# Kernel tuning notes

Hardware: AMD Instinct MI355X
Metric: run time of the kernel (lower is better)

## Reference

```python
import jax, jax.numpy as jnp
import numpy as np

B = 16384      # batch of (user, item) interactions
N = 819200     # total packed implicit-history items (~50 per user)
U = 100000     # num_users
I = 100000     # num_items
D = 64         # emb_dim


def setup_inputs() -> dict:
    key = jax.random.key(0)
    ks = jax.random.split(key, 8)
    user_ids = jax.random.randint(ks[0], (B,), 0, U)
    item_ids = jax.random.randint(ks[1], (B,), 0, I)
    offsets = jnp.sort(jax.random.randint(ks[2], (B,), 0, N)).at[0].set(0)
    flat_implicit = jax.random.randint(ks[3], (N,), 0, I)
    user_emb = 0.1 * jax.random.normal(ks[4], (U, D), dtype=jnp.float32)
    item_emb = 0.1 * jax.random.normal(ks[5], (I, D), dtype=jnp.float32)
    implicit_item_emb = 0.1 * jax.random.normal(ks[6], (I, D), dtype=jnp.float32)
    user_bias = jnp.zeros((U, 1), dtype=jnp.float32)
    item_bias = jnp.zeros((I, 1), dtype=jnp.float32)
    global_bias = jnp.zeros((1,), dtype=jnp.float32)
    return {"user_ids": user_ids, "item_ids": item_ids, "offsets": offsets,
            "flat_implicit": flat_implicit, "user_emb": user_emb,
            "item_emb": item_emb, "implicit_item_emb": implicit_item_emb,
            "user_bias": user_bias, "item_bias": item_bias,
            "global_bias": global_bias}


def reference(user_ids, item_ids, offsets, flat_implicit, user_emb, item_emb,
              implicit_item_emb, user_bias, item_bias, global_bias):
    n = flat_implicit.shape[0]
    b = offsets.shape[0]
    u = user_emb[user_ids]                       # [B, D]
    i = item_emb[item_ids]                       # [B, D]
    imp = implicit_item_emb[flat_implicit]       # [N, D]
    # ragged segment ids from start offsets (empty segments get no rows)
    seg_ids = jnp.searchsorted(offsets, jnp.arange(n), side="right") - 1
    summed = jax.ops.segment_sum(imp, seg_ids, num_segments=b)  # [B, D]
    sizes = jnp.diff(jnp.concatenate([offsets, jnp.array([n], dtype=offsets.dtype)]))
    norm = jnp.where(sizes > 0, jnp.sqrt(sizes.astype(jnp.float32)), 1.0)
    final_user = u + summed / norm[:, None]
    dot = jnp.sum(final_user * i, axis=1)        # [B]
    pred = dot + user_bias[user_ids][:, 0] + item_bias[item_ids][:, 0] + global_bias
    return pred
```

## Files before the change

### kernel.cpp

```cpp
#include <hip/hip_runtime.h>
#include <math.h>


#define WAVES_PER_BLOCK 4

__global__ __launch_bounds__(256) void svdpp_kernel(
    const int* __restrict__ user_ids,
    const int* __restrict__ item_ids,
    const int* __restrict__ offsets,
    const int* __restrict__ flat_implicit,
    const float* __restrict__ user_emb,
    const float* __restrict__ item_emb,
    const float* __restrict__ imp_emb,
    const float* __restrict__ user_bias,
    const float* __restrict__ item_bias,
    const float* __restrict__ global_bias,
    float* __restrict__ out,
    int B, int N)
{
    const int wave = threadIdx.x >> 6;
    const int lane = threadIdx.x & 63;
    const int b = blockIdx.x * WAVES_PER_BLOCK + wave;
    if (b >= B) return;

    const int sub = lane >> 4;
    const int l16 = lane & 15;

    const int start = offsets[b];
    const int end   = (b + 1 < B) ? offsets[b + 1] : N;
    const int n     = end - start;

    const int user = user_ids[b];
    const int item = item_ids[b];

    const float4 i4 = ((const float4*)(item_emb + (size_t)item * 64))[l16];

    float4 acc = make_float4(0.f, 0.f, 0.f, 0.f);

    int j = start + sub;
    for (; j + 12 < end; j += 16) {
        const int idx0 = flat_implicit[j];
        const int idx1 = flat_implicit[j + 4];
        const int idx2 = flat_implicit[j + 8];
        const int idx3 = flat_implicit[j + 12];
        const float4 v0 = ((const float4*)(imp_emb + (size_t)idx0 * 64))[l16];
        const float4 v1 = ((const float4*)(imp_emb + (size_t)idx1 * 64))[l16];
        const float4 v2 = ((const float4*)(imp_emb + (size_t)idx2 * 64))[l16];
        const float4 v3 = ((const float4*)(imp_emb + (size_t)idx3 * 64))[l16];
        acc.x += v0.x + v1.x + v2.x + v3.x;
        acc.y += v0.y + v1.y + v2.y + v3.y;
        acc.z += v0.z + v1.z + v2.z + v3.z;
        acc.w += v0.w + v1.w + v2.w + v3.w;
    }
    for (; j < end; j += 4) {
        const int idx = flat_implicit[j];
        const float4 v = ((const float4*)(imp_emb + (size_t)idx * 64))[l16];
        acc.x += v.x; acc.y += v.y; acc.z += v.z; acc.w += v.w;
    }

    float ds = acc.x * i4.x + acc.y * i4.y + acc.z * i4.z + acc.w * i4.w;

    const float u_c = user_emb[(size_t)user * 64 + lane];
    const float i_c = item_emb[(size_t)item * 64 + lane];
    float dui = u_c * i_c;

    #pragma unroll
    for (int off = 32; off >= 1; off >>= 1) {
        ds  += __shfl_xor(ds,  off, 64);
        dui += __shfl_xor(dui, off, 64);
    }

    if (lane == 0) {
        const float norm = (n > 0) ? sqrtf((float)n) : 1.0f;
        out[b] = dui + ds / norm + user_bias[user] + item_bias[item]
               + global_bias[0];
    }
}

extern "C" void kernel_launch(void* const* d_in, const int* in_sizes, int n_in,
                              void* d_out, int out_size, void* d_ws, size_t ws_size,
                              hipStream_t stream) {
    const int*   user_ids      = (const int*)  d_in[0];
    const int*   item_ids      = (const int*)  d_in[1];
    const int*   offsets       = (const int*)  d_in[2];
    const int*   flat_implicit = (const int*)  d_in[3];
    const float* user_emb      = (const float*)d_in[4];
    const float* item_emb      = (const float*)d_in[5];
    const float* imp_emb       = (const float*)d_in[6];
    const float* user_bias     = (const float*)d_in[7];
    const float* item_bias     = (const float*)d_in[8];
    const float* global_bias   = (const float*)d_in[9];
    float* out = (float*)d_out;

    const int B = in_sizes[0];
    const int N = in_sizes[3];

    const int grid = (B + WAVES_PER_BLOCK - 1) / WAVES_PER_BLOCK;
    svdpp_kernel<<<grid, WAVES_PER_BLOCK * 64, 0, stream>>>(
        user_ids, item_ids, offsets, flat_implicit,
        user_emb, item_emb, imp_emb,
        user_bias, item_bias, global_bias,
        out, B, N);
}
```

Before: 146.9 us.

## Split each segment across two chunks with atomic accumulation into output

Each batch row's implicit-history segment is now divided into two halves handled by separate waves along a second grid dimension, and their partial dot products are combined with atomicAdd into an output zeroed by a memset. The aim is to raise parallelism and cut the per-wave serial gather chain for long, uneven segments. The tail loop is replaced by fixed unrolled remainder steps. In exchange it adds a memset launch, an atomic per chunk, a reload of the item row per chunk, and summation order that can vary between runs.

```diff
diff --git a/kernel.cpp b/kernel.cpp
--- a/kernel.cpp
+++ b/kernel.cpp
@@ -3,6 +3,7 @@
 
 
 #define WAVES_PER_BLOCK 4
+#define CHUNKS 2
 
 __global__ __launch_bounds__(256) void svdpp_kernel(
     const int* __restrict__ user_ids,
@@ -21,6 +22,7 @@
     const int wave = threadIdx.x >> 6;
     const int lane = threadIdx.x & 63;
     const int b = blockIdx.x * WAVES_PER_BLOCK + wave;
+    const int c = blockIdx.y;
     if (b >= B) return;
 
     const int sub = lane >> 4;
@@ -30,15 +32,17 @@
     const int end   = (b + 1 < B) ? offsets[b + 1] : N;
     const int n     = end - start;
 
-    const int user = user_ids[b];
+    const int cs = start + (int)(((long long)n * c) / CHUNKS);
+    const int ce = start + (int)(((long long)n * (c + 1)) / CHUNKS);
+
     const int item = item_ids[b];
 
     const float4 i4 = ((const float4*)(item_emb + (size_t)item * 64))[l16];
 
     float4 acc = make_float4(0.f, 0.f, 0.f, 0.f);
 
-    int j = start + sub;
-    for (; j + 12 < end; j += 16) {
+    int j = cs + sub;
+    for (; j + 12 < ce; j += 16) {
         const int idx0 = flat_implicit[j];
         const int idx1 = flat_implicit[j + 4];
         const int idx2 = flat_implicit[j + 8];
@@ -52,28 +56,45 @@
         acc.z += v0.z + v1.z + v2.z + v3.z;
         acc.w += v0.w + v1.w + v2.w + v3.w;
     }
-    for (; j < end; j += 4) {
+    if (j + 4 < ce) {
+        const int idx0 = flat_implicit[j];
+        const int idx1 = flat_implicit[j + 4];
+        const float4 v0 = ((const float4*)(imp_emb + (size_t)idx0 * 64))[l16];
+        const float4 v1 = ((const float4*)(imp_emb + (size_t)idx1 * 64))[l16];
+        acc.x += v0.x + v1.x; acc.y += v0.y + v1.y;
+        acc.z += v0.z + v1.z; acc.w += v0.w + v1.w;
+        j += 8;
+    }
+    if (j < ce) {
         const int idx = flat_implicit[j];
         const float4 v = ((const float4*)(imp_emb + (size_t)idx * 64))[l16];
         acc.x += v.x; acc.y += v.y; acc.z += v.z; acc.w += v.w;
     }
 
-    float ds = acc.x * i4.x + acc.y * i4.y + acc.z * i4.z + acc.w * i4.w;
+    float val = acc.x * i4.x + acc.y * i4.y + acc.z * i4.z + acc.w * i4.w;
 
-    const float u_c = user_emb[(size_t)user * 64 + lane];
-    const float i_c = item_emb[(size_t)item * 64 + lane];
-    float dui = u_c * i_c;
+    float dui = 0.f;
+    if (c == 0) {
+        const int user = user_ids[b];
+        const float u_c = user_emb[(size_t)user * 64 + lane];
+        const float i_c = item_emb[(size_t)item * 64 + lane];
+        dui = u_c * i_c;
+    }
 
     #pragma unroll
     for (int off = 32; off >= 1; off >>= 1) {
-        ds  += __shfl_xor(ds,  off, 64);
+        val += __shfl_xor(val, off, 64);
         dui += __shfl_xor(dui, off, 64);
     }
 
     if (lane == 0) {
         const float norm = (n > 0) ? sqrtf((float)n) : 1.0f;
-        out[b] = dui + ds / norm + user_bias[user] + item_bias[item]
-               + global_bias[0];
+        float contrib = val / norm;
+        if (c == 0) {
+            const int user = user_ids[b];
+            contrib += dui + user_bias[user] + item_bias[item] + global_bias[0];
+        }
+        atomicAdd(out + b, contrib);
     }
 }
 
@@ -95,7 +116,9 @@
     const int B = in_sizes[0];
     const int N = in_sizes[3];
 
-    const int grid = (B + WAVES_PER_BLOCK - 1) / WAVES_PER_BLOCK;
+    hipMemsetAsync(out, 0, (size_t)B * sizeof(float), stream);
+
+    dim3 grid((B + WAVES_PER_BLOCK - 1) / WAVES_PER_BLOCK, CHUNKS);
     svdpp_kernel<<<grid, WAVES_PER_BLOCK * 64, 0, stream>>>(
         user_ids, item_ids, offsets, flat_implicit,
         user_emb, item_emb, imp_emb,
```

Result: no change. 146.7 us (-0.1%).
